# Kernel optimization log

Hardware: AMD Instinct MI355X
Metric: run time of the kernel (lower is better)

Reference implementation:

```python
import jax, jax.numpy as jnp
import numpy as np

NUM_EXPERTS = 8
TOP_K = 2


def setup_inputs() -> dict:
    key = jax.random.key(0)
    ks = jax.random.split(key, 5)
    B, S, D, F, E = 4, 2048, 1024, 3584, NUM_EXPERTS
    scale = 0.02
    return {
        "hidden_states": jax.random.normal(ks[0], (B, S, D), dtype=jnp.float32),
        "gate_w": jax.random.normal(ks[1], (E, D), dtype=jnp.float32) * scale,
        "w1": jax.random.normal(ks[2], (E, D, F), dtype=jnp.float32) * scale,
        "w3": jax.random.normal(ks[3], (E, D, F), dtype=jnp.float32) * scale,
        "w2": jax.random.normal(ks[4], (E, F, D), dtype=jnp.float32) * scale,
    }


def reference(hidden_states, gate_w, w1, w3, w2):
    B, S, D = hidden_states.shape
    E = gate_w.shape[0]
    x = hidden_states.reshape(-1, D)  # [T, D]

    # Router: logits -> softmax -> top-k -> renormalize
    router_logits = x @ gate_w.T  # [T, E]
    routing_probs = jax.nn.softmax(router_logits, axis=-1)
    top_w, top_idx = jax.lax.top_k(routing_probs, TOP_K)  # [T, K]
    top_w = top_w / jnp.sum(top_w, axis=-1, keepdims=True)

    # Per-token weight for each expert (0 if not selected): [T, E]
    expert_weight = jnp.sum(
        jax.nn.one_hot(top_idx, E, dtype=x.dtype) * top_w[..., None], axis=1
    )

    # Dense masked dispatch: small fixed loop over experts (E=8), SwiGLU MLP.
    out = jnp.zeros_like(x)
    for e in range(E):
        h = jax.nn.silu(x @ w1[e]) * (x @ w3[e])  # [T, F]
        out = out + expert_weight[:, e:e + 1] * (h @ w2[e])  # [T, D]

    return out.reshape(B, S, D), router_logits
```

## Files before the change

### kernel.cpp

```cpp
#include <hip/hip_runtime.h>
#include <stdint.h>

#define T_TOKENS 8192
#define DDIM 1024
#define FDIM 3584
#define NEXP 8

#define MAXT1 72
#define MAXT2 136

typedef _Float16 f16x8 __attribute__((ext_vector_type(8)));
typedef float f32x4 __attribute__((ext_vector_type(4)));

__device__ __forceinline__ void gload16(const void* g, void* l) {
  __builtin_amdgcn_global_load_lds(
      (const __attribute__((address_space(1))) void*)g,
      (__attribute__((address_space(3))) void*)l, 16, 0, 0);
}

#define FENCE asm volatile("" ::: "memory")
#define BARRIER do { FENCE; __builtin_amdgcn_s_barrier(); FENCE; } while (0)

#define GPHASE(q, ...) {                                                                                     \
    f16x8 a0  = *(const f16x8*)&LA[(wm + ((q) * 2)     * 16 + l15) * 64 + pc0];                              \
    f16x8 a0k = *(const f16x8*)&LA[(wm + ((q) * 2)     * 16 + l15) * 64 + pc1];                              \
    f16x8 a1  = *(const f16x8*)&LA[(wm + ((q) * 2 + 1) * 16 + l15) * 64 + pc0];                              \
    f16x8 a1k = *(const f16x8*)&LA[(wm + ((q) * 2 + 1) * 16 + l15) * 64 + pc1];                              \
    __VA_ARGS__;                                                                                             \
    BARRIER;                                                                                                 \
    __builtin_amdgcn_s_setprio(1);                                                                           \
    _Pragma("unroll")                                                                                        \
    for (int j = 0; j < 4; j++) {                                                                            \
      acc[(q) * 2][j]     = __builtin_amdgcn_mfma_f32_16x16x32_f16(a0,  bf[0][j], acc[(q) * 2][j], 0, 0, 0); \
      acc[(q) * 2 + 1][j] = __builtin_amdgcn_mfma_f32_16x16x32_f16(a1,  bf[0][j], acc[(q) * 2 + 1][j], 0, 0, 0); \
    }                                                                                                        \
    _Pragma("unroll")                                                                                        \
    for (int j = 0; j < 4; j++) {                                                                            \
      acc[(q) * 2][j]     = __builtin_amdgcn_mfma_f32_16x16x32_f16(a0k, bf[1][j], acc[(q) * 2][j], 0, 0, 0); \
      acc[(q) * 2 + 1][j] = __builtin_amdgcn_mfma_f32_16x16x32_f16(a1k, bf[1][j], acc[(q) * 2 + 1][j], 0, 0, 0); \
    }                                                                                                        \
    __builtin_amdgcn_s_setprio(0);                                                                           \
    BARRIER;                                                                                                 \
  }

__global__ __launch_bounds__(256) void router_kernel(
    const float* __restrict__ x, const float* __restrict__ gw,
    float* __restrict__ logits_out, int* __restrict__ counts,
    int* __restrict__ tok_idx, float* __restrict__ tok_w,
    int2* __restrict__ tok_ref, _Float16* __restrict__ xh) {
  int t = blockIdx.x * 4 + (threadIdx.x >> 6);
  int lane = threadIdx.x & 63;
  const float* xr = x + (size_t)t * DDIM;
  float acc[NEXP];
#pragma unroll
  for (int e = 0; e < NEXP; e++) acc[e] = 0.f;
  for (int c = 0; c < DDIM / 64; c++) {
    float xv = xr[c * 64 + lane];
    xh[(size_t)t * DDIM + c * 64 + lane] = (_Float16)xv;
#pragma unroll
    for (int e = 0; e < NEXP; e++) acc[e] += xv * gw[e * DDIM + c * 64 + lane];
  }
#pragma unroll
  for (int e = 0; e < NEXP; e++) {
    for (int off = 32; off > 0; off >>= 1) acc[e] += __shfl_xor(acc[e], off, 64);
  }
  if (lane == 0) {
    float m = acc[0];
    for (int e = 1; e < NEXP; e++) m = fmaxf(m, acc[e]);
    float p[NEXP];
    for (int e = 0; e < NEXP; e++) p[e] = expf(acc[e] - m);
    int e1 = 0;
    for (int e = 1; e < NEXP; e++) if (p[e] > p[e1]) e1 = e;
    int e2 = (e1 == 0) ? 1 : 0;
    for (int e = 0; e < NEXP; e++) { if (e == e1) continue; if (p[e] > p[e2]) e2 = e; }
    float wsum = p[e1] + p[e2];
    float w1v = p[e1] / wsum, w2v = p[e2] / wsum;
    for (int e = 0; e < NEXP; e++) logits_out[(size_t)t * NEXP + e] = acc[e];
    int pos1 = atomicAdd(&counts[e1], 1);
    tok_idx[e1 * T_TOKENS + pos1] = t; tok_w[e1 * T_TOKENS + pos1] = w1v;
    int pos2 = atomicAdd(&counts[e2], 1);
    tok_idx[e2 * T_TOKENS + pos2] = t; tok_w[e2 * T_TOKENS + pos2] = w2v;
    tok_ref[t] = make_int2((e1 << 13) | pos1, (e2 << 13) | pos2);
  }
}

__global__ void prefix_kernel(const int* __restrict__ counts, int* __restrict__ offsets,
                              int* __restrict__ sched1, int* __restrict__ sched2) {
  if (threadIdx.x == 0) {
    int s = 0, n1 = 0, n2 = 0;
    for (int e = 0; e < NEXP; e++) {
      offsets[e] = s;
      int cc = counts[e];
      int nt1 = (cc + 255) / 256;
      for (int i = 0; i < nt1; i++) sched1[n1++] = (e << 16) | i;
      int nt2 = (cc + 127) / 128;
      for (int i = 0; i < nt2; i++) sched2[n2++] = (e << 16) | i;
      s += cc;
    }
    offsets[NEXP] = s;
    for (; n1 < MAXT1; n1++) sched1[n1] = -1;
    for (; n2 < MAXT2; n2++) sched2[n2] = -1;
  }
}

__global__ __launch_bounds__(256) void transpose_f16_kernel(
    const float* __restrict__ in, _Float16* __restrict__ out, int R, int C) {
  __shared__ _Float16 lt[64][72];
  size_t esz = (size_t)R * C;
  in += (size_t)blockIdx.z * esz;
  out += (size_t)blockIdx.z * esz;
  int r0 = blockIdx.y * 64, c0 = blockIdx.x * 64;
  int t = threadIdx.x;
  int r = t & 63, q = t >> 6;
  const float* src = in + (size_t)(r0 + r) * C + c0 + q * 16;
  float4 v0 = ((const float4*)src)[0];
  float4 v1 = ((const float4*)src)[1];
  float4 v2 = ((const float4*)src)[2];
  float4 v3 = ((const float4*)src)[3];
  _Float16 f[16] = {
      (_Float16)v0.x, (_Float16)v0.y, (_Float16)v0.z, (_Float16)v0.w,
      (_Float16)v1.x, (_Float16)v1.y, (_Float16)v1.z, (_Float16)v1.w,
      (_Float16)v2.x, (_Float16)v2.y, (_Float16)v2.z, (_Float16)v2.w,
      (_Float16)v3.x, (_Float16)v3.y, (_Float16)v3.z, (_Float16)v3.w};
#pragma unroll
  for (int j = 0; j < 16; j++) lt[q * 16 + j][r] = f[j];
  __syncthreads();
  _Float16* dst = out + (size_t)(c0 + r) * R + r0 + q * 16;
  *(f16x8*)dst       = *(const f16x8*)&lt[r][q * 16];
  *(f16x8*)(dst + 8) = *(const f16x8*)&lt[r][q * 16 + 8];
}

__global__ __launch_bounds__(512, 2) void gemm1_kernel(
    const _Float16* __restrict__ xh, const _Float16* __restrict__ w1t,
    const _Float16* __restrict__ w3t, const int* __restrict__ counts,
    const int* __restrict__ offsets, const int* __restrict__ tok_idx,
    const int* __restrict__ sched, _Float16* __restrict__ h) {
  int sc = sched[blockIdx.y];
  if (sc < 0) return;
  int e = sc >> 16, rt = sc & 0xFFFF;
  int cnt = counts[e];
  int ct = blockIdx.x;
  int off = offsets[e];

  __shared__ _Float16 lds[2][32768];

  int tid = threadIdx.x, lane = tid & 63, wv = tid >> 6;
  int rsub = lane >> 3, p8 = lane & 7, cch = p8 ^ rsub;

  int R0 = (wv & 1) * 128 + (wv >> 1) * 32;
  const _Float16* aS[4];
#pragma unroll
  for (int g = 0; g < 4; g++) {
    int ir = rt * 256 + R0 + g * 8 + rsub;
    if (ir >= cnt) ir = cnt - 1;
    int tok = tok_idx[e * T_TOKENS + ir];
    aS[g] = xh + (size_t)tok * DDIM + cch * 8;
  }
  const _Float16* wsel = (wv & 1) ? w3t : w1t;
  const _Float16* bS[4];
#pragma unroll
  for (int g = 0; g < 4; g++) {
    size_t row = (size_t)e * FDIM + (size_t)ct * 128 + (wv >> 1) * 32 + g * 8 + rsub;
    bS[g] = wsel + row * DDIM + cch * 8;
  }

  {
    _Float16* Lb = lds[0];
#pragma unroll
    for (int g = 0; g < 4; g++) gload16(aS[g], Lb + R0 * 64 + g * 512);
#pragma unroll
    for (int g = 0; g < 4; g++) gload16(bS[g], Lb + 16384 + wv * 2048 + g * 512);
  }
  {
    _Float16* Lb = lds[1];
#pragma unroll
    for (int g = 0; g < 4; g++) gload16(aS[g] + 64, Lb + R0 * 64 + g * 512);
#pragma unroll
    for (int g = 0; g < 4; g++) gload16(bS[g] + 64, Lb + 16384 + wv * 2048 + g * 512);
  }
#pragma unroll
  for (int g = 0; g < 4; g++) { aS[g] += 128; bS[g] += 128; }

  f32x4 acc[8][4];
  f32x4 zero = {0.f, 0.f, 0.f, 0.f};
#pragma unroll
  for (int m = 0; m < 8; m++)
#pragma unroll
    for (int j = 0; j < 4; j++) acc[m][j] = zero;

  int wm = (wv >> 2) * 128, wc = wv & 3;
  int l15 = lane & 15, qv = lane >> 4, x7 = l15 & 7;
  int pc0 = (qv ^ x7) * 8, pc1 = ((4 + qv) ^ x7) * 8;
  f16x8 bf[2][4];

  for (int t = 0; t < DDIM / 64; t++) {
    if (t < DDIM / 64 - 1) asm volatile("s_waitcnt vmcnt(8)" ::: "memory");
    else                   asm volatile("s_waitcnt vmcnt(0)" ::: "memory");
    BARRIER;
    const _Float16* LA = lds[t & 1];
    const _Float16* LB = LA + 16384;
    _Float16* LbA = lds[t & 1] + R0 * 64;
    _Float16* LbB = lds[t & 1] + 16384 + wv * 2048;
    bool pf = (t < DDIM / 64 - 2);
    GPHASE(0,
      _Pragma("unroll")
      for (int j = 0; j < 4; j++) bf[0][j] = *(const f16x8*)&LB[(wc * 64 + j * 16 + l15) * 64 + pc0];
      _Pragma("unroll")
      for (int j = 0; j < 4; j++) bf[1][j] = *(const f16x8*)&LB[(wc * 64 + j * 16 + l15) * 64 + pc1];
    );
    GPHASE(1, if (pf) { gload16(bS[0], LbB); gload16(bS[1], LbB + 512); });
    GPHASE(2, if (pf) { gload16(bS[2], LbB + 1024); gload16(bS[3], LbB + 1536); });
    GPHASE(3, if (pf && wv < 6) { gload16(aS[0], LbA); gload16(aS[1], LbA + 512); });
    if (pf) {
      if (wv < 6) { gload16(aS[2], LbA + 1024); gload16(aS[3], LbA + 1536); }
      else {
        gload16(aS[0], LbA);        gload16(aS[1], LbA + 512);
        gload16(aS[2], LbA + 1024); gload16(aS[3], LbA + 1536);
      }
    }
#pragma unroll
    for (int g = 0; g < 4; g++) { aS[g] += 64; bS[g] += 64; }
  }

  int q4 = qv * 4;
#pragma unroll
  for (int m = 0; m < 8; m++) {
#pragma unroll
    for (int r = 0; r < 4; r++) {
      int row = rt * 256 + wm + m * 16 + q4 + r;
      if (row >= cnt) continue;
      _Float16* hrow = h + (size_t)(off + row) * FDIM + (size_t)ct * 128 + wc * 32;
#pragma unroll
      for (int j = 0; j < 2; j++) {
        float a = acc[m][j][r];
        float b = acc[m][j + 2][r];
        float hv = (a / (1.f + __expf(-a))) * b;
        hrow[j * 16 + l15] = (_Float16)hv;
      }
    }
  }
}

__global__ __launch_bounds__(256, 2) void gemm2_kernel(
    const _Float16* __restrict__ h, const _Float16* __restrict__ w2t,
    const int* __restrict__ counts, const int* __restrict__ offsets,
    const float* __restrict__ tok_w, const int* __restrict__ sched,
    _Float16* __restrict__ part) {
  int sc = sched[blockIdx.y];
  if (sc < 0) return;
  int e = sc >> 16, rt = sc & 0xFFFF;
  int cnt = counts[e];
  int ct = blockIdx.x;
  int off = offsets[e];

  __shared__ _Float16 lds[2][16384];

  int tid = threadIdx.x, lane = tid & 63, wv = tid >> 6;
  int rsub = lane >> 3, p8 = lane & 7, cch = p8 ^ rsub;

  const _Float16* aS[4];
  const _Float16* bS[4];
#pragma unroll
  for (int g = 0; g < 4; g++) {
    int r = wv * 32 + g * 8 + rsub;
    aS[g] = h + (size_t)(off + rt * 128 + r) * FDIM + cch * 8;
    bS[g] = w2t + ((size_t)e * DDIM + (size_t)ct * 128 + r) * FDIM + cch * 8;
  }

  {
    _Float16* Lb = lds[0];
#pragma unroll
    for (int g = 0; g < 4; g++) gload16(aS[g], Lb + wv * 2048 + g * 512);
#pragma unroll
    for (int g = 0; g < 4; g++) gload16(bS[g], Lb + 8192 + wv * 2048 + g * 512);
  }
  {
    _Float16* Lb = lds[1];
#pragma unroll
    for (int g = 0; g < 4; g++) gload16(aS[g] + 64, Lb + wv * 2048 + g * 512);
#pragma unroll
    for (int g = 0; g < 4; g++) gload16(bS[g] + 64, Lb + 8192 + wv * 2048 + g * 512);
  }
#pragma unroll
  for (int g = 0; g < 4; g++) { aS[g] += 128; bS[g] += 128; }

  f32x4 acc[4][4];
  f32x4 zero = {0.f, 0.f, 0.f, 0.f};
#pragma unroll
  for (int m = 0; m < 4; m++)
#pragma unroll
    for (int j = 0; j < 4; j++) acc[m][j] = zero;

  int wm = (wv >> 1) * 64, wn = (wv & 1) * 64;
  int l15 = lane & 15, qv = lane >> 4, x7 = l15 & 7;
  int pc0 = (qv ^ x7) * 8, pc1 = ((4 + qv) ^ x7) * 8;
  f16x8 bf[2][4];

  for (int t = 0; t < FDIM / 64; t++) {
    if (t < FDIM / 64 - 1) asm volatile("s_waitcnt vmcnt(8)" ::: "memory");
    else                   asm volatile("s_waitcnt vmcnt(0)" ::: "memory");
    BARRIER;
    const _Float16* LA = lds[t & 1];
    const _Float16* LB = LA + 8192;
    _Float16* LbA = lds[t & 1] + wv * 2048;
    _Float16* LbB = lds[t & 1] + 8192 + wv * 2048;
    bool pf = (t < FDIM / 64 - 2);
    GPHASE(0,
      _Pragma("unroll")
      for (int j = 0; j < 4; j++) bf[0][j] = *(const f16x8*)&LB[(wn + j * 16 + l15) * 64 + pc0];
      _Pragma("unroll")
      for (int j = 0; j < 4; j++) bf[1][j] = *(const f16x8*)&LB[(wn + j * 16 + l15) * 64 + pc1];
    );
    GPHASE(1, if (pf) {
      gload16(bS[0], LbB);        gload16(bS[1], LbB + 512);
      gload16(bS[2], LbB + 1024); gload16(bS[3], LbB + 1536);
    });
    if (pf) {
      gload16(aS[0], LbA);        gload16(aS[1], LbA + 512);
      gload16(aS[2], LbA + 1024); gload16(aS[3], LbA + 1536);
    }
#pragma unroll
    for (int g = 0; g < 4; g++) { aS[g] += 64; bS[g] += 64; }
  }

  int q4 = qv * 4;
#pragma unroll
  for (int m = 0; m < 4; m++) {
#pragma unroll
    for (int r = 0; r < 4; r++) {
      int row = rt * 128 + wm + m * 16 + q4 + r;
      if (row >= cnt) continue;
      float wgt = tok_w[e * T_TOKENS + row];
      _Float16* prow = part + (size_t)(off + row) * DDIM + (size_t)ct * 128 + wn;
#pragma unroll
      for (int j = 0; j < 4; j++)
        prow[j * 16 + l15] = (_Float16)(acc[m][j][r] * wgt);
    }
  }
}

__global__ __launch_bounds__(256) void gather_kernel(
    const _Float16* __restrict__ part, const int2* __restrict__ tok_ref,
    const int* __restrict__ offsets, float* __restrict__ out) {
  int i = blockIdx.x * 256 + threadIdx.x;
  int t = i >> 7;
  int dc = (i & 127) * 8;
  int2 ref = tok_ref[t];
  int sa = offsets[ref.x >> 13] + (ref.x & 8191);
  int sb = offsets[ref.y >> 13] + (ref.y & 8191);
  f16x8 pa = *(const f16x8*)(part + (size_t)sa * DDIM + dc);
  f16x8 pb = *(const f16x8*)(part + (size_t)sb * DDIM + dc);
  float* dst = out + (size_t)t * DDIM + dc;
#pragma unroll
  for (int j = 0; j < 8; j++) dst[j] = (float)pa[j] + (float)pb[j];
}

extern "C" void kernel_launch(void* const* d_in, const int* in_sizes, int n_in,
                              void* d_out, int out_size, void* d_ws, size_t ws_size,
                              hipStream_t stream) {
  const float* x  = (const float*)d_in[0];
  const float* gw = (const float*)d_in[1];
  const float* w1 = (const float*)d_in[2];
  const float* w3 = (const float*)d_in[3];
  const float* w2 = (const float*)d_in[4];
  float* out = (float*)d_out;
  float* logits = out + (size_t)T_TOKENS * DDIM;

  char* ws = (char*)d_ws;
  const size_t MB = 1024 * 1024;
  int* counts  = (int*)ws;
  int* offsets = (int*)(ws + 64);
  int* sched1  = (int*)(ws + 128);
  int* sched2  = (int*)(ws + 512);
  int* tok_idx = (int*)(ws + 2048);
  float* tok_w = (float*)(ws + 2048 + 262144);
  int2* tok_ref = (int2*)(ws + 2048 + 2 * 262144);
  _Float16* xh  = (_Float16*)(ws + 1 * MB);
  _Float16* w1t = (_Float16*)(ws + 17 * MB);
  _Float16* w3t = (_Float16*)(ws + 73 * MB);
  _Float16* w2t = (_Float16*)(ws + 129 * MB);
  _Float16* h   = (_Float16*)(ws + 185 * MB);
  _Float16* part = (_Float16*)(ws + 304 * MB);

  hipMemsetAsync(counts, 0, 256, stream);

  router_kernel<<<T_TOKENS / 4, 256, 0, stream>>>(x, gw, logits, counts, tok_idx, tok_w, tok_ref, xh);
  prefix_kernel<<<1, 64, 0, stream>>>(counts, offsets, sched1, sched2);

  transpose_f16_kernel<<<dim3(FDIM / 64, DDIM / 64, NEXP), 256, 0, stream>>>(w1, w1t, DDIM, FDIM);
  transpose_f16_kernel<<<dim3(FDIM / 64, DDIM / 64, NEXP), 256, 0, stream>>>(w3, w3t, DDIM, FDIM);
  transpose_f16_kernel<<<dim3(DDIM / 64, FDIM / 64, NEXP), 256, 0, stream>>>(w2, w2t, FDIM, DDIM);

  gemm1_kernel<<<dim3(FDIM / 128, MAXT1), 512, 0, stream>>>(xh, w1t, w3t, counts, offsets, tok_idx, sched1, h);
  gemm2_kernel<<<dim3(DDIM / 128, MAXT2), 256, 0, stream>>>(h, w2t, counts, offsets, tok_w, sched2, part);
  gather_kernel<<<T_TOKENS * DDIM / 8 / 256, 256, 0, stream>>>(part, tok_ref, offsets, out);
}
```

Baseline: 1.012 ms.

## Widen gemm2 tile to 128x256 with 512 threads and pad gemm1 grid

gemm2 moves from 256-thread blocks with 128x128 output tiles to 512-thread blocks covering 128 rows by 256 columns, so each loaded A (h) tile is reused across twice as many output columns. The A loads are split across waves and issued in different phases, and the vmcnt wait is adjusted to match. A-row indices are now clamped to the valid token count. gemm1's grid x dimension is padded from 28 to 32 with an early exit for the extra blocks, which only adds a few idle blocks. The larger tile uses more LDS and registers per block, which may lower occupancy.

```diff
diff --git a/kernel.cpp b/kernel.cpp
--- a/kernel.cpp
+++ b/kernel.cpp
@@ -135,11 +135,12 @@
     const _Float16* __restrict__ w3t, const int* __restrict__ counts,
     const int* __restrict__ offsets, const int* __restrict__ tok_idx,
     const int* __restrict__ sched, _Float16* __restrict__ h) {
+  int ct = blockIdx.x;
+  if (ct >= FDIM / 128) return;
   int sc = sched[blockIdx.y];
   if (sc < 0) return;
   int e = sc >> 16, rt = sc & 0xFFFF;
   int cnt = counts[e];
-  int ct = blockIdx.x;
   int off = offsets[e];
 
   __shared__ _Float16 lds[2][32768];
@@ -241,7 +242,7 @@
   }
 }
 
-__global__ __launch_bounds__(256, 2) void gemm2_kernel(
+__global__ __launch_bounds__(512, 2) void gemm2_kernel(
     const _Float16* __restrict__ h, const _Float16* __restrict__ w2t,
     const int* __restrict__ counts, const int* __restrict__ offsets,
     const float* __restrict__ tok_w, const int* __restrict__ sched,
@@ -253,36 +254,43 @@
   int ct = blockIdx.x;
   int off = offsets[e];
 
-  __shared__ _Float16 lds[2][16384];
+  __shared__ _Float16 lds[2][24576];
 
   int tid = threadIdx.x, lane = tid & 63, wv = tid >> 6;
   int rsub = lane >> 3, p8 = lane & 7, cch = p8 ^ rsub;
 
-  const _Float16* aS[4];
+  const _Float16* aS[2];
+#pragma unroll
+  for (int g = 0; g < 2; g++) {
+    int ir = rt * 128 + wv * 16 + g * 8 + rsub;
+    if (ir >= cnt) ir = cnt - 1;
+    aS[g] = h + (size_t)(off + ir) * FDIM + cch * 8;
+  }
   const _Float16* bS[4];
 #pragma unroll
   for (int g = 0; g < 4; g++) {
-    int r = wv * 32 + g * 8 + rsub;
-    aS[g] = h + (size_t)(off + rt * 128 + r) * FDIM + cch * 8;
-    bS[g] = w2t + ((size_t)e * DDIM + (size_t)ct * 128 + r) * FDIM + cch * 8;
+    size_t row = (size_t)e * DDIM + (size_t)ct * 256 + wv * 32 + g * 8 + rsub;
+    bS[g] = w2t + row * FDIM + cch * 8;
   }
 
   {
     _Float16* Lb = lds[0];
 #pragma unroll
-    for (int g = 0; g < 4; g++) gload16(aS[g], Lb + wv * 2048 + g * 512);
+    for (int g = 0; g < 2; g++) gload16(aS[g], Lb + wv * 1024 + g * 512);
 #pragma unroll
     for (int g = 0; g < 4; g++) gload16(bS[g], Lb + 8192 + wv * 2048 + g * 512);
   }
   {
     _Float16* Lb = lds[1];
 #pragma unroll
-    for (int g = 0; g < 4; g++) gload16(aS[g] + 64, Lb + wv * 2048 + g * 512);
+    for (int g = 0; g < 2; g++) gload16(aS[g] + 64, Lb + wv * 1024 + g * 512);
 #pragma unroll
     for (int g = 0; g < 4; g++) gload16(bS[g] + 64, Lb + 8192 + wv * 2048 + g * 512);
   }
 #pragma unroll
-  for (int g = 0; g < 4; g++) { aS[g] += 128; bS[g] += 128; }
+  for (int g = 0; g < 2; g++) aS[g] += 128;
+#pragma unroll
+  for (int g = 0; g < 4; g++) bS[g] += 128;
 
   f32x4 acc[4][4];
   f32x4 zero = {0.f, 0.f, 0.f, 0.f};
@@ -291,36 +299,38 @@
 #pragma unroll
     for (int j = 0; j < 4; j++) acc[m][j] = zero;
 
-  int wm = (wv >> 1) * 64, wn = (wv & 1) * 64;
+  int wm = (wv >> 2) * 64, wc = wv & 3;
   int l15 = lane & 15, qv = lane >> 4, x7 = l15 & 7;
   int pc0 = (qv ^ x7) * 8, pc1 = ((4 + qv) ^ x7) * 8;
   f16x8 bf[2][4];
 
+  int aPh1 = (wv >> 1) & 1;
+
   for (int t = 0; t < FDIM / 64; t++) {
-    if (t < FDIM / 64 - 1) asm volatile("s_waitcnt vmcnt(8)" ::: "memory");
+    if (t < FDIM / 64 - 1) asm volatile("s_waitcnt vmcnt(6)" ::: "memory");
     else                   asm volatile("s_waitcnt vmcnt(0)" ::: "memory");
     BARRIER;
     const _Float16* LA = lds[t & 1];
     const _Float16* LB = LA + 8192;
-    _Float16* LbA = lds[t & 1] + wv * 2048;
+    _Float16* LbA = lds[t & 1] + wv * 1024;
     _Float16* LbB = lds[t & 1] + 8192 + wv * 2048;
     bool pf = (t < FDIM / 64 - 2);
     GPHASE(0,
       _Pragma("unroll")
-      for (int j = 0; j < 4; j++) bf[0][j] = *(const f16x8*)&LB[(wn + j * 16 + l15) * 64 + pc0];
+      for (int j = 0; j < 4; j++) bf[0][j] = *(const f16x8*)&LB[(wc * 64 + j * 16 + l15) * 64 + pc0];
       _Pragma("unroll")
-      for (int j = 0; j < 4; j++) bf[1][j] = *(const f16x8*)&LB[(wn + j * 16 + l15) * 64 + pc1];
+      for (int j = 0; j < 4; j++) bf[1][j] = *(const f16x8*)&LB[(wc * 64 + j * 16 + l15) * 64 + pc1];
     );
     GPHASE(1, if (pf) {
       gload16(bS[0], LbB);        gload16(bS[1], LbB + 512);
       gload16(bS[2], LbB + 1024); gload16(bS[3], LbB + 1536);
+      if (!aPh1) { gload16(aS[0], LbA); gload16(aS[1], LbA + 512); }
     });
-    if (pf) {
-      gload16(aS[0], LbA);        gload16(aS[1], LbA + 512);
-      gload16(aS[2], LbA + 1024); gload16(aS[3], LbA + 1536);
-    }
-#pragma unroll
-    for (int g = 0; g < 4; g++) { aS[g] += 64; bS[g] += 64; }
+    if (pf && aPh1) { gload16(aS[0], LbA); gload16(aS[1], LbA + 512); }
+#pragma unroll
+    for (int g = 0; g < 2; g++) aS[g] += 64;
+#pragma unroll
+    for (int g = 0; g < 4; g++) bS[g] += 64;
   }
 
   int q4 = qv * 4;
@@ -331,7 +341,7 @@
       int row = rt * 128 + wm + m * 16 + q4 + r;
       if (row >= cnt) continue;
       float wgt = tok_w[e * T_TOKENS + row];
-      _Float16* prow = part + (size_t)(off + row) * DDIM + (size_t)ct * 128 + wn;
+      _Float16* prow = part + (size_t)(off + row) * DDIM + (size_t)ct * 256 + wc * 64;
 #pragma unroll
       for (int j = 0; j < 4; j++)
         prow[j * 16 + l15] = (_Float16)(acc[m][j][r] * wgt);
@@ -391,7 +401,7 @@
   transpose_f16_kernel<<<dim3(FDIM / 64, DDIM / 64, NEXP), 256, 0, stream>>>(w3, w3t, DDIM, FDIM);
   transpose_f16_kernel<<<dim3(DDIM / 64, FDIM / 64, NEXP), 256, 0, stream>>>(w2, w2t, FDIM, DDIM);
 
-  gemm1_kernel<<<dim3(FDIM / 128, MAXT1), 512, 0, stream>>>(xh, w1t, w3t, counts, offsets, tok_idx, sched1, h);
-  gemm2_kernel<<<dim3(DDIM / 128, MAXT2), 256, 0, stream>>>(h, w2t, counts, offsets, tok_w, sched2, part);
+  gemm1_kernel<<<dim3(32, MAXT1), 512, 0, stream>>>(xh, w1t, w3t, counts, offsets, tok_idx, sched1, h);
+  gemm2_kernel<<<dim3(DDIM / 256, MAXT2), 512, 0, stream>>>(h, w2t, counts, offsets, tok_w, sched2, part);
   gather_kernel<<<T_TOKENS * DDIM / 8 / 256, 256, 0, stream>>>(part, tok_ref, offsets, out);
 }
```

Result: slower. 1.067 ms (+5.4%).
